# Optimization experiments

Measured on AMD Instinct MI355X. Metric: run time of the kernel, lower is better.

Reference implementation:

```python
import jax, jax.numpy as jnp
import numpy as np

K1 = 20
K2 = 6
LAMBDA = 0.3
MARGIN = 0.03


def _pairwise_sq(x, y):
    # squared euclidean distance (standard re-ID pairwise_distance, clamped at 0)
    xx = jnp.sum(x * x, axis=1)
    yy = jnp.sum(y * y, axis=1)
    d = xx[:, None] + yy[None, :] - 2.0 * (x @ y.T)
    return jnp.maximum(d, 0.0)


def _recip_mask(R, k):
    # boolean (N,N) mask: M[i,j]=True iff j is in i's top-(k+1) AND i is in j's top-(k+1)
    N = R.shape[0]
    topk = R[:, : k + 1]                       # (N, k+1)
    back = topk[topk]                          # (N, k+1, k+1)
    cond = jnp.any(back == jnp.arange(N)[:, None, None], axis=2)  # (N, k+1)
    rows = jnp.broadcast_to(jnp.arange(N)[:, None], topk.shape)
    return jnp.zeros((N, N), bool).at[rows, topk].set(cond)


def _rerank_dist(feat):
    n = feat.shape[0]
    feats = jnp.concatenate([feat, feat], axis=0)      # feat1 == feat2 == inputs
    N = feats.shape[0]
    D = _pairwise_sq(feats, feats)                     # (N, N)
    original = D.T                                     # original_dist (symmetric)
    # eval_type=True: gallery columns replaced by global max before ranking
    maxv = D.max()
    dist = jnp.concatenate([D[:, :n], jnp.full((N, N - n), maxv, D.dtype)], axis=1)
    R = jnp.argsort(dist, axis=1)                      # stable argsort
    K = _recip_mask(R, K1)                             # k-reciprocal sets
    Khalf = _recip_mask(R, int(round(K1 / 2)))         # half-size reciprocal sets
    Kf = K.astype(jnp.float32)
    Khf = Khalf.astype(jnp.float32)
    inter = Kf @ Khf.T                                 # inter[i,j] = |Khalf[j] & K[i]|
    sizes = Khf.sum(axis=1)                            # |Khalf[j]|
    expand = K & (inter > (2.0 / 3.0) * sizes[None, :])
    E = K | ((expand.astype(jnp.float32) @ Khf) > 0)   # expanded reciprocal sets
    W = jnp.exp(-original) * E
    s = W.sum(axis=1, keepdims=True)
    V = W / jnp.where(s == 0, 1.0, s)                  # rows with empty sets stay zero
    # local query expansion over top-k2 neighbors
    V = V[R[:, :K2]].mean(axis=1)                      # (N, N)

    def jrow(vi):
        # sum_j min(V[i,j], V[t,j]) over all t; zeros contribute nothing (matches invIndex)
        tmin = jnp.sum(jnp.minimum(vi[None, :], V), axis=1)   # (N,)
        return 1.0 - tmin / (2.0 - tmin)

    jac = jax.lax.map(jax.checkpoint(jrow), V[:n])     # (n, N)
    final = jac * (1.0 - LAMBDA) + original[:n] * LAMBDA
    return final[:, n:]                                # (n, n)


def setup_inputs() -> dict:
    key = jax.random.key(0)
    k1, k2 = jax.random.split(key)
    x = jax.random.normal(k1, (1024, 2048), jnp.float32)
    x = x / jnp.linalg.norm(x, axis=1, keepdims=True)  # L2-normalized re-ID embeddings
    targets = jax.random.randint(k2, (1024,), 0, 128)
    return {"inputs": x, "targets": targets}


def reference(inputs, targets):
    dist = _rerank_dist(inputs)                        # (n, n)
    mask = targets[:, None] == targets[None, :]
    dist_ap = jnp.where(mask, dist, -jnp.inf).max(axis=1)
    dist_an = jnp.where(mask, jnp.inf, dist).min(axis=1)
    # MarginRankingLoss(dist_an, dist_ap, y=1) = mean(relu(dist_ap - dist_an + margin))
    loss = jnp.mean(jax.nn.relu(dist_ap - dist_an + MARGIN))
    return (loss, dist, dist_ap, dist_an)
```

## Files before the change

### kernel.cpp

```cpp
#include <hip/hip_runtime.h>

#define N 1024
#define DIM 2048

typedef unsigned long long u64;

__device__ __forceinline__ u64 umin64(u64 a, u64 b){ return a < b ? a : b; }

__device__ __forceinline__ void tri_map(int lid, int* by, int* bx){
  int y = (int)((sqrtf(8.0f * lid + 1.0f) - 1.0f) * 0.5f);
  while ((y + 1) * (y + 2) / 2 <= lid) y++;
  while (y * (y + 1) / 2 > lid) y--;
  *by = y;
  *bx = lid - y * (y + 1) / 2;
}

__global__ __launch_bounds__(256) void rownorm_kernel(const float* __restrict__ x, float* __restrict__ xx){
  int i = blockIdx.x, t = threadIdx.x;
  const float4* row = (const float4*)(x + (size_t)i * DIM);
  float s = 0.f;
  #pragma unroll
  for (int q = 0; q < 2; q++){
    float4 v = row[t + q*256];
    s += v.x*v.x + v.y*v.y + v.z*v.z + v.w*v.w;
  }
  #pragma unroll
  for (int off = 32; off > 0; off >>= 1) s += __shfl_down(s, off);
  __shared__ float sm[4];
  if ((t & 63) == 0) sm[t >> 6] = s;
  __syncthreads();
  if (t == 0) xx[i] = sm[0] + sm[1] + sm[2] + sm[3];
}

__global__ __launch_bounds__(256) void gemm_split_kernel(const float* __restrict__ x,
    float* __restrict__ p0, float* __restrict__ p1, int kc){
  __shared__ __align__(16) float As[32][64];
  __shared__ __align__(16) float Bs[32][64];
  int by, bx; tri_map(blockIdx.x, &by, &bx);
  int z = blockIdx.y;
  int t = threadIdx.x;
  int tx = t & 15, ty = t >> 4;
  int i0 = by * 64, j0 = bx * 64;
  int kbase = z * kc;
  int nslab = kc >> 5;
  int row0 = t >> 3, kq = t & 7;
  int sw = kq << 3;

  float4 fa0 = *(const float4*)&x[(size_t)(i0+row0)*DIM    + kbase + kq*4];
  float4 fa1 = *(const float4*)&x[(size_t)(i0+row0+32)*DIM + kbase + kq*4];
  float4 fb0 = *(const float4*)&x[(size_t)(j0+row0)*DIM    + kbase + kq*4];
  float4 fb1 = *(const float4*)&x[(size_t)(j0+row0+32)*DIM + kbase + kq*4];

  float acc[4][4] = {};
  for (int s = 0; s < nslab; s++){
    {
      float va0[4] = {fa0.x, fa0.y, fa0.z, fa0.w};
      float va1[4] = {fa1.x, fa1.y, fa1.z, fa1.w};
      float vb0[4] = {fb0.x, fb0.y, fb0.z, fb0.w};
      float vb1[4] = {fb1.x, fb1.y, fb1.z, fb1.w};
      #pragma unroll
      for (int e2 = 0; e2 < 4; e2++){
        As[kq*4+e2][row0 ^ sw]      = va0[e2];
        As[kq*4+e2][(row0+32) ^ sw] = va1[e2];
        Bs[kq*4+e2][row0 ^ sw]      = vb0[e2];
        Bs[kq*4+e2][(row0+32) ^ sw] = vb1[e2];
      }
    }
    __syncthreads();
    if (s + 1 < nslab){
      int k0 = kbase + (s+1)*32;
      fa0 = *(const float4*)&x[(size_t)(i0+row0)*DIM    + k0 + kq*4];
      fa1 = *(const float4*)&x[(size_t)(i0+row0+32)*DIM + k0 + kq*4];
      fb0 = *(const float4*)&x[(size_t)(j0+row0)*DIM    + k0 + kq*4];
      fb1 = *(const float4*)&x[(size_t)(j0+row0+32)*DIM + k0 + kq*4];
    }
    #pragma unroll
    for (int kk = 0; kk < 32; kk++){
      int swk = (kk >> 2) << 3;
      float4 a4 = *(const float4*)&As[kk][(ty*4) ^ swk];
      float4 b4 = *(const float4*)&Bs[kk][(tx*4) ^ swk];
      float av[4] = {a4.x, a4.y, a4.z, a4.w};
      float bv[4] = {b4.x, b4.y, b4.z, b4.w};
      #pragma unroll
      for (int r = 0; r < 4; r++){
        #pragma unroll
        for (int c = 0; c < 4; c++) acc[r][c] = fmaf(av[r], bv[c], acc[r][c]);
      }
    }
    __syncthreads();
  }
  float* P = (z == 0) ? p0 : p1 + (size_t)(z - 1) * N * N;
  #pragma unroll
  for (int r = 0; r < 4; r++){
    #pragma unroll
    for (int c = 0; c < 4; c++){
      int i = i0 + ty*4 + r, j = j0 + tx*4 + c;
      P[(size_t)i * N + j] = acc[r][c];
    }
  }
}

__global__ __launch_bounds__(256) void gemm_combine_kernel(
    const float* __restrict__ p0, const float* __restrict__ p1,
    int nsplit, const float* __restrict__ xx, float* __restrict__ D){
  __shared__ float Ts[32][68];
  int by, bx; tri_map(blockIdx.x, &by, &bx);
  int h = blockIdx.y;
  int t = threadIdx.x;
  int tc = t & 15, tr = t >> 4;
  int i0 = by * 64 + h * 32, j0 = bx * 64;
  float4 xj = *(const float4*)&xx[j0 + tc*4];
  #pragma unroll
  for (int rr = 0; rr < 2; rr++){
    int r = tr*2 + rr;
    int i = i0 + r;
    size_t off = (size_t)i * N + j0 + tc*4;
    float4 s = *(const float4*)&p0[off];
    for (int z = 1; z < nsplit; z++){
      float4 q = *(const float4*)&p1[(size_t)(z-1)*N*N + off];
      s.x += q.x; s.y += q.y; s.z += q.z; s.w += q.w;
    }
    float xxi = xx[i];
    float4 o;
    o.x = xxi + xj.x - 2.0f*s.x; o.x = (o.x > 0.f) ? o.x : 0.f;
    o.y = xxi + xj.y - 2.0f*s.y; o.y = (o.y > 0.f) ? o.y : 0.f;
    o.z = xxi + xj.z - 2.0f*s.z; o.z = (o.z > 0.f) ? o.z : 0.f;
    o.w = xxi + xj.w - 2.0f*s.w; o.w = (o.w > 0.f) ? o.w : 0.f;
    *(float4*)&D[off] = o;
    Ts[r][tc*4+0] = o.x; Ts[r][tc*4+1] = o.y;
    Ts[r][tc*4+2] = o.z; Ts[r][tc*4+3] = o.w;
  }
  if (by == bx) return;
  __syncthreads();
  int tc2 = t & 7, jr0 = t >> 3;
  #pragma unroll
  for (int e = 0; e < 2; e++){
    int c = jr0 + e*32;
    float4 o;
    o.x = Ts[tc2*4+0][c];
    o.y = Ts[tc2*4+1][c];
    o.z = Ts[tc2*4+2][c];
    o.w = Ts[tc2*4+3][c];
    *(float4*)&D[(size_t)(j0 + c) * N + i0 + tc2*4] = o;
  }
}

__global__ __launch_bounds__(64) void topk_kernel(const float* __restrict__ D, int* __restrict__ T){
  int i = blockIdx.x, t = threadIdx.x;
  const float* row = D + (size_t)i * N;
  u64 key[16];
  #pragma unroll
  for (int q = 0; q < 4; q++){
    int l0 = t*4 + q*256;
    float4 f = *(const float4*)&row[l0];
    key[q*4+0] = ((u64)__float_as_uint(f.x) << 32) | (unsigned)(l0+0);
    key[q*4+1] = ((u64)__float_as_uint(f.y) << 32) | (unsigned)(l0+1);
    key[q*4+2] = ((u64)__float_as_uint(f.z) << 32) | (unsigned)(l0+2);
    key[q*4+3] = ((u64)__float_as_uint(f.w) << 32) | (unsigned)(l0+3);
  }
  for (int it = 0; it < 21; ++it){
    u64 m = key[0];
    #pragma unroll
    for (int q = 1; q < 16; q++) m = umin64(m, key[q]);
    #pragma unroll
    for (int off = 1; off < 64; off <<= 1) m = umin64(m, __shfl_xor(m, off));
    if (t == 0) T[i*21 + it] = (int)(m & 0xffffffffull);
    #pragma unroll
    for (int q = 0; q < 16; q++) if (key[q] == m) key[q] = ~0ull;
  }
}

__global__ __launch_bounds__(64) void recip_kernel(const int* __restrict__ T,
                                                   u64* __restrict__ Kb, u64* __restrict__ Khb){
  int i = blockIdx.x, t = threadIdx.x;
  __shared__ u64 kb[16], khb[16];
  if (t < 16){ kb[t] = 0; khb[t] = 0; }
  __syncthreads();
  if (t < 21){
    int j = T[i*21 + t];
    bool r21 = false, r11 = false;
    for (int p = 0; p < 21; p++){
      if (T[j*21 + p] == i){ r21 = true; if (p < 11) r11 = true; }
    }
    if (r21) atomicOr(&kb[j >> 6], 1ull << (j & 63));
    if (t < 11 && r11) atomicOr(&khb[j >> 6], 1ull << (j & 63));
  }
  __syncthreads();
  if (t < 16){ Kb[i*16 + t] = kb[t]; Khb[i*16 + t] = khb[t]; }
}

__global__ __launch_bounds__(64) void expand_kernel(const u64* __restrict__ Kb,
                                                    const u64* __restrict__ Khb,
                                                    u64* __restrict__ Eb){
  int i = blockIdx.x;
  int lane = threadIdx.x;
  __shared__ u64 er[16];
  __shared__ int js[32];
  __shared__ int njs;
  if (lane == 0) njs = 0;
  __syncthreads();
  if (lane < 16){
    u64 w = Kb[i*16 + lane];
    er[lane] = w;
    while (w){
      int bit = __ffsll((long long)w) - 1;
      w &= w - 1;
      int pos = atomicAdd(&njs, 1);
      js[pos] = lane*64 + bit;
    }
  }
  __syncthreads();
  if (lane < njs){
    int j = js[lane];
    int inter = 0, sz = 0;
    #pragma unroll
    for (int w = 0; w < 16; w++){
      u64 kh = Khb[(size_t)j*16 + w];
      u64 kw = Kb[(size_t)i*16 + w];
      inter += __popcll(kw & kh);
      sz += __popcll(kh);
    }
    if (3*inter > 2*sz){
      #pragma unroll
      for (int w = 0; w < 16; w++){
        u64 kh = Khb[(size_t)j*16 + w];
        if (kh) atomicOr(&er[w], kh);
      }
    }
  }
  __syncthreads();
  if (lane < 16) Eb[i*16 + lane] = er[lane];
}

__global__ __launch_bounds__(256) void v_kernel(const float* __restrict__ Dm,
                                                const u64* __restrict__ Eb,
                                                float* __restrict__ V){
  int i = blockIdx.x, t = threadIdx.x;
  float w[4];
  #pragma unroll
  for (int q = 0; q < 4; q++){
    int l = t + q*256;
    u64 word = Eb[i*16 + (l >> 6)];
    float e = expf(-Dm[(size_t)i * N + l]);
    w[q] = ((word >> (l & 63)) & 1ull) ? e : 0.f;
  }
  float s = w[0] + w[1] + w[2] + w[3];
  #pragma unroll
  for (int off = 32; off > 0; off >>= 1) s += __shfl_down(s, off);
  __shared__ float sm[4];
  __shared__ float stot;
  if ((t & 63) == 0) sm[t >> 6] = s;
  __syncthreads();
  if (t == 0){ float S = sm[0] + sm[1] + sm[2] + sm[3]; stot = (S == 0.f) ? 1.f : S; }
  __syncthreads();
  float denom = stot;
  #pragma unroll
  for (int q = 0; q < 4; q++){
    int l = t + q*256;
    V[(size_t)i * N + l] = w[q] / denom;
  }
}

__global__ __launch_bounds__(256) void vbar_kernel(const float* __restrict__ V,
                                                   const int* __restrict__ T,
                                                   float* __restrict__ Vb){
  int i = blockIdx.x, t = threadIdx.x;
  int t6[6];
  #pragma unroll
  for (int p = 0; p < 6; p++) t6[p] = T[i*21 + p];
  #pragma unroll
  for (int q = 0; q < 4; q++){
    int l = t + q*256;
    float s = 0.f;
    #pragma unroll
    for (int p = 0; p < 6; p++) s += V[(size_t)t6[p] * N + l];
    Vb[(size_t)i * N + l] = s / 6.0f;
  }
}

__global__ __launch_bounds__(256) void jac_split_kernel(const float* __restrict__ Vb,
    float* __restrict__ p0, float* __restrict__ p1, int kc){
  __shared__ __align__(16) float As[32][64];
  __shared__ __align__(16) float Bs[32][64];
  int by, bx; tri_map(blockIdx.x, &by, &bx);
  int z = blockIdx.y;
  int t = threadIdx.x;
  int tx = t & 15, ty = t >> 4;
  int i0 = by * 64, j0 = bx * 64;
  int kbase = z * kc;
  int nslab = kc >> 5;
  int row0 = t >> 3, kq = t & 7;
  int sw = kq << 3;

  float4 fa0 = *(const float4*)&Vb[(size_t)(i0+row0)*N    + kbase + kq*4];
  float4 fa1 = *(const float4*)&Vb[(size_t)(i0+row0+32)*N + kbase + kq*4];
  float4 fb0 = *(const float4*)&Vb[(size_t)(j0+row0)*N    + kbase + kq*4];
  float4 fb1 = *(const float4*)&Vb[(size_t)(j0+row0+32)*N + kbase + kq*4];

  float acc[4][4] = {};
  for (int s = 0; s < nslab; s++){
    {
      float va0[4] = {fa0.x, fa0.y, fa0.z, fa0.w};
      float va1[4] = {fa1.x, fa1.y, fa1.z, fa1.w};
      float vb0[4] = {fb0.x, fb0.y, fb0.z, fb0.w};
      float vb1[4] = {fb1.x, fb1.y, fb1.z, fb1.w};
      #pragma unroll
      for (int e2 = 0; e2 < 4; e2++){
        As[kq*4+e2][row0 ^ sw]      = va0[e2];
        As[kq*4+e2][(row0+32) ^ sw] = va1[e2];
        Bs[kq*4+e2][row0 ^ sw]      = vb0[e2];
        Bs[kq*4+e2][(row0+32) ^ sw] = vb1[e2];
      }
    }
    __syncthreads();
    if (s + 1 < nslab){
      int k0 = kbase + (s+1)*32;
      fa0 = *(const float4*)&Vb[(size_t)(i0+row0)*N    + k0 + kq*4];
      fa1 = *(const float4*)&Vb[(size_t)(i0+row0+32)*N + k0 + kq*4];
      fb0 = *(const float4*)&Vb[(size_t)(j0+row0)*N    + k0 + kq*4];
      fb1 = *(const float4*)&Vb[(size_t)(j0+row0+32)*N + k0 + kq*4];
    }
    #pragma unroll
    for (int kk = 0; kk < 32; kk++){
      int swk = (kk >> 2) << 3;
      float4 a4 = *(const float4*)&As[kk][(ty*4) ^ swk];
      float4 b4 = *(const float4*)&Bs[kk][(tx*4) ^ swk];
      float av[4] = {a4.x, a4.y, a4.z, a4.w};
      float bv[4] = {b4.x, b4.y, b4.z, b4.w};
      #pragma unroll
      for (int r = 0; r < 4; r++){
        #pragma unroll
        for (int c = 0; c < 4; c++) acc[r][c] += fminf(av[r], bv[c]);
      }
    }
    __syncthreads();
  }
  float* P = (z == 0) ? p0 : p1 + (size_t)(z - 1) * N * N;
  #pragma unroll
  for (int r = 0; r < 4; r++){
    #pragma unroll
    for (int c = 0; c < 4; c++){
      int i = i0 + ty*4 + r, j = j0 + tx*4 + c;
      P[(size_t)i * N + j] = acc[r][c];
    }
  }
}

__global__ __launch_bounds__(256) void jac_combine_kernel(
    const float* __restrict__ p0, const float* __restrict__ p1,
    int nsplit, float* __restrict__ Dm){
  __shared__ float Ts[32][68];
  int by, bx; tri_map(blockIdx.x, &by, &bx);
  int h = blockIdx.y;
  int t = threadIdx.x;
  int tc = t & 15, tr = t >> 4;
  int i0 = by * 64 + h * 32, j0 = bx * 64;
  #pragma unroll
  for (int rr = 0; rr < 2; rr++){
    int r = tr*2 + rr;
    int i = i0 + r;
    size_t off = (size_t)i * N + j0 + tc*4;
    float4 s = *(const float4*)&p0[off];
    for (int z = 1; z < nsplit; z++){
      float4 q = *(const float4*)&p1[(size_t)(z-1)*N*N + off];
      s.x += q.x; s.y += q.y; s.z += q.z; s.w += q.w;
    }
    float4 d0 = *(const float4*)&Dm[off];
    float4 o;
    o.x = 0.7f * (1.0f - s.x / (2.0f - s.x)) + 0.3f * d0.x;
    o.y = 0.7f * (1.0f - s.y / (2.0f - s.y)) + 0.3f * d0.y;
    o.z = 0.7f * (1.0f - s.z / (2.0f - s.z)) + 0.3f * d0.z;
    o.w = 0.7f * (1.0f - s.w / (2.0f - s.w)) + 0.3f * d0.w;
    *(float4*)&Dm[off] = o;
    Ts[r][tc*4+0] = o.x; Ts[r][tc*4+1] = o.y;
    Ts[r][tc*4+2] = o.z; Ts[r][tc*4+3] = o.w;
  }
  if (by == bx) return;
  __syncthreads();
  int tc2 = t & 7, jr0 = t >> 3;
  #pragma unroll
  for (int e = 0; e < 2; e++){
    int c = jr0 + e*32;
    float4 o;
    o.x = Ts[tc2*4+0][c];
    o.y = Ts[tc2*4+1][c];
    o.z = Ts[tc2*4+2][c];
    o.w = Ts[tc2*4+3][c];
    *(float4*)&Dm[(size_t)(j0 + c) * N + i0 + tc2*4] = o;
  }
}

__global__ __launch_bounds__(256) void apan_kernel(const float* __restrict__ Dm,
                                                   const int* __restrict__ tg,
                                                   float* __restrict__ ap, float* __restrict__ an){
  int i = blockIdx.x, t = threadIdx.x;
  int ti = tg[i];
  float mx = -3.402823466e38f, mn = 3.402823466e38f;
  #pragma unroll
  for (int q = 0; q < 4; q++){
    int l = t + q*256;
    float v = Dm[(size_t)i * N + l];
    if (tg[l] == ti) mx = fmaxf(mx, v); else mn = fminf(mn, v);
  }
  #pragma unroll
  for (int off = 32; off > 0; off >>= 1){
    mx = fmaxf(mx, __shfl_down(mx, off));
    mn = fminf(mn, __shfl_down(mn, off));
  }
  __shared__ float smx[4], smn[4];
  if ((t & 63) == 0){ smx[t >> 6] = mx; smn[t >> 6] = mn; }
  __syncthreads();
  if (t == 0){
    ap[i] = fmaxf(fmaxf(smx[0], smx[1]), fmaxf(smx[2], smx[3]));
    an[i] = fminf(fminf(smn[0], smn[1]), fminf(smn[2], smn[3]));
  }
}

__global__ __launch_bounds__(256) void loss_kernel(const float* __restrict__ ap,
                                                   const float* __restrict__ an,
                                                   float* __restrict__ out){
  int t = threadIdx.x;
  float s = 0.f;
  #pragma unroll
  for (int q = 0; q < 4; q++){
    int l = t + q*256;
    s += fmaxf(ap[l] - an[l] + 0.03f, 0.f);
  }
  #pragma unroll
  for (int off = 32; off > 0; off >>= 1) s += __shfl_down(s, off);
  __shared__ float sm[4];
  if ((t & 63) == 0) sm[t >> 6] = s;
  __syncthreads();
  if (t == 0) out[0] = (sm[0] + sm[1] + sm[2] + sm[3]) / 1024.0f;
}

static const size_t XX_OFF  = 0;
static const size_t T_OFF   = 4096;
static const size_t KB_OFF  = 90112;
static const size_t KHB_OFF = 221184;
static const size_t EB_OFF  = 352256;
static const size_t V_OFF   = 483328;
static const size_t VB_OFF  = 4677632;
static const size_t P1_OFF  = 8871936;
static const size_t NN4     = 4194304;

extern "C" void kernel_launch(void* const* d_in, const int* in_sizes, int n_in,
                              void* d_out, int out_size, void* d_ws, size_t ws_size,
                              hipStream_t stream){
  const float* x  = (const float*)d_in[0];
  const int*   tg = (const int*)d_in[1];
  float* out = (float*)d_out;
  char* ws = (char*)d_ws;
  if (ws_size < P1_OFF) return;

  float* xx  = (float*)(ws + XX_OFF);
  int*   T   = (int*)(ws + T_OFF);
  u64*   Kb  = (u64*)(ws + KB_OFF);
  u64*   Khb = (u64*)(ws + KHB_OFF);
  u64*   Eb  = (u64*)(ws + EB_OFF);
  float* V   = (float*)(ws + V_OFF);
  float* Vb  = (float*)(ws + VB_OFF);

  float* dist = out + 1;
  float* ap   = out + 1 + (size_t)N*N;
  float* an   = ap + N;

  size_t avail = ws_size - P1_OFF;
  int nsplit = (avail >= 7*NN4) ? 8 : (avail >= 3*NN4) ? 4 : (avail >= 1*NN4) ? 2 : 1;
  float* P0 = V;
  float* P1 = (float*)(ws + P1_OFF);

  rownorm_kernel     <<<N, 256, 0, stream>>>(x, xx);
  gemm_split_kernel  <<<dim3(136, nsplit), 256, 0, stream>>>(x, P0, P1, DIM/nsplit);
  gemm_combine_kernel<<<dim3(136, 2), 256, 0, stream>>>(P0, P1, nsplit, xx, dist);
  topk_kernel        <<<N, 64, 0, stream>>>(dist, T);
  recip_kernel       <<<N, 64, 0, stream>>>(T, Kb, Khb);
  expand_kernel      <<<N, 64, 0, stream>>>(Kb, Khb, Eb);
  v_kernel           <<<N, 256, 0, stream>>>(dist, Eb, V);
  vbar_kernel        <<<N, 256, 0, stream>>>(V, T, Vb);
  jac_split_kernel   <<<dim3(136, nsplit), 256, 0, stream>>>(Vb, P0, P1, N/nsplit);
  jac_combine_kernel <<<dim3(136, 2), 256, 0, stream>>>(P0, P1, nsplit, dist);
  apan_kernel        <<<N, 256, 0, stream>>>(dist, tg, ap, an);
  loss_kernel        <<<1, 256, 0, stream>>>(ap, an, out);
}
```

Baseline: 144.3 us.

## Compute Jaccard term with a sparse inverted index instead of a dense min-sum

Replaces the dense split min-sum pass over the full N×N×N space with a sparse path. It builds per-row support bitmasks for the query-expanded V, then a column-wise inverted index (via atomics), and then accumulates min(V[i,k], V[j,k]) only over nonzero entries in shared memory. The aim is to skip the large amount of arithmetic on zero entries. In exchange it adds three kernels, a memset, atomic index construction, and per-nonzero block-wide barriers. The old dense path is kept as a fallback when the workspace is too small.

```diff
diff --git a/kernel.cpp b/kernel.cpp
--- a/kernel.cpp
+++ b/kernel.cpp
@@ -278,6 +278,84 @@
   }
 }
 
+__global__ __launch_bounds__(64) void vbs_kernel(const int* __restrict__ T,
+                                                 const u64* __restrict__ Eb,
+                                                 u64* __restrict__ VbS){
+  int i = blockIdx.x, t = threadIdx.x;
+  if (t >= 16) return;
+  u64 o = 0;
+  #pragma unroll
+  for (int p = 0; p < 6; p++){
+    int tj = T[i*21 + p];
+    o |= Eb[(size_t)tj*16 + t];
+  }
+  VbS[i*16 + t] = o;
+}
+
+__global__ __launch_bounds__(64) void colbuild_kernel(const float* __restrict__ Vb,
+                                                      const u64* __restrict__ VbS,
+                                                      int* __restrict__ colCnt,
+                                                      int* __restrict__ colJ,
+                                                      float* __restrict__ colV){
+  int j = blockIdx.x, lane = threadIdx.x;
+  if (lane >= 16) return;
+  u64 b = VbS[j*16 + lane];
+  while (b){
+    int k = lane*64 + __ffsll((long long)b) - 1;
+    b &= b - 1;
+    int pos = atomicAdd(&colCnt[k], 1);
+    colJ[k*1024 + pos] = j;
+    colV[k*1024 + pos] = Vb[(size_t)j*N + k];
+  }
+}
+
+__global__ __launch_bounds__(256) void jac_sparse_kernel(const float* __restrict__ Vb,
+                                                         const u64* __restrict__ VbS,
+                                                         const int* __restrict__ colCnt,
+                                                         const int* __restrict__ colJ,
+                                                         const float* __restrict__ colV,
+                                                         float* __restrict__ Dm){
+  int i = blockIdx.x, t = threadIdx.x;
+  __shared__ float viRow[N];
+  __shared__ float tmp[N];
+  __shared__ u64 sbits[16];
+  #pragma unroll
+  for (int q = 0; q < 4; q++){
+    int l = t + q*256;
+    viRow[l] = Vb[(size_t)i*N + l];
+    tmp[l] = 0.f;
+  }
+  if (t < 16) sbits[t] = VbS[i*16 + t];
+  __syncthreads();
+  for (int w = 0; w < 16; w++){
+    u64 b = sbits[w];
+    while (b){
+      int k = w*64 + __ffsll((long long)b) - 1;
+      b &= b - 1;
+      float vik = viRow[k];
+      int len = colCnt[k];
+      for (int base = 0; base < len; base += 256){
+        int idx = base + t;
+        if (idx < len){
+          int j = colJ[k*1024 + idx];
+          float vj = colV[k*1024 + idx];
+          tmp[j] += fminf(vik, vj);
+        }
+      }
+      __syncthreads();
+    }
+  }
+  __syncthreads();
+  #pragma unroll
+  for (int q = 0; q < 4; q++){
+    int l = t + q*256;
+    float tm = tmp[l];
+    size_t off = (size_t)i*N + l;
+    float d0 = Dm[off];
+    Dm[off] = 0.7f * (1.0f - tm / (2.0f - tm)) + 0.3f * d0;
+  }
+}
+
 __global__ __launch_bounds__(256) void jac_split_kernel(const float* __restrict__ Vb,
     float* __restrict__ p0, float* __restrict__ p1, int kc){
   __shared__ __align__(16) float As[32][64];
@@ -443,6 +521,11 @@
 static const size_t VB_OFF  = 4677632;
 static const size_t P1_OFF  = 8871936;
 static const size_t NN4     = 4194304;
+static const size_t CJ_REL   = 0;
+static const size_t CV_REL   = 4194304;
+static const size_t CC_REL   = 8388608;
+static const size_t VBS_REL  = 8392704;
+static const size_t SPARSE_NEED = 8523776;
 
 extern "C" void kernel_launch(void* const* d_in, const int* in_sizes, int n_in,
                               void* d_out, int out_size, void* d_ws, size_t ws_size,
@@ -470,6 +553,12 @@
   float* P0 = V;
   float* P1 = (float*)(ws + P1_OFF);
 
+  bool use_sparse = (avail >= SPARSE_NEED);
+  int*   colJ   = (int*)(ws + P1_OFF + CJ_REL);
+  float* colV   = (float*)(ws + P1_OFF + CV_REL);
+  int*   colCnt = (int*)(ws + P1_OFF + CC_REL);
+  u64*   VbS    = (u64*)(ws + P1_OFF + VBS_REL);
+
   rownorm_kernel     <<<N, 256, 0, stream>>>(x, xx);
   gemm_split_kernel  <<<dim3(136, nsplit), 256, 0, stream>>>(x, P0, P1, DIM/nsplit);
   gemm_combine_kernel<<<dim3(136, 2), 256, 0, stream>>>(P0, P1, nsplit, xx, dist);
@@ -478,8 +567,15 @@
   expand_kernel      <<<N, 64, 0, stream>>>(Kb, Khb, Eb);
   v_kernel           <<<N, 256, 0, stream>>>(dist, Eb, V);
   vbar_kernel        <<<N, 256, 0, stream>>>(V, T, Vb);
-  jac_split_kernel   <<<dim3(136, nsplit), 256, 0, stream>>>(Vb, P0, P1, N/nsplit);
-  jac_combine_kernel <<<dim3(136, 2), 256, 0, stream>>>(P0, P1, nsplit, dist);
+  if (use_sparse){
+    vbs_kernel       <<<N, 64, 0, stream>>>(T, Eb, VbS);
+    hipMemsetAsync(colCnt, 0, 1024*sizeof(int), stream);
+    colbuild_kernel  <<<N, 64, 0, stream>>>(Vb, VbS, colCnt, colJ, colV);
+    jac_sparse_kernel<<<N, 256, 0, stream>>>(Vb, VbS, colCnt, colJ, colV, dist);
+  } else {
+    jac_split_kernel <<<dim3(136, nsplit), 256, 0, stream>>>(Vb, P0, P1, N/nsplit);
+    jac_combine_kernel<<<dim3(136, 2), 256, 0, stream>>>(P0, P1, nsplit, dist);
+  }
   apan_kernel        <<<N, 256, 0, stream>>>(dist, tg, ap, an);
   loss_kernel        <<<1, 256, 0, stream>>>(ap, an, out);
 }
```

After: 180.3 us. 1.25x slower.
